# Kernel optimization log

Measured on AMD Instinct MI355X. Metric: run time of the kernel, lower is better.

## Reference

```python
import jax, jax.numpy as jnp
import numpy as np

N_CONTEXT = 8
N_ANS = 8


def _g_mlp(x, Wg1, bg1, Wg2, bg2, Wg3, bg3):
    # 3-layer relation MLP G, applied per object pair
    h = jax.nn.relu(x @ Wg1 + bg1)
    h = jax.nn.relu(h @ Wg2 + bg2)
    return jax.nn.relu(h @ Wg3 + bg3)


def setup_inputs() -> dict:
    key = jax.random.key(0)
    ks = jax.random.split(key, 12)
    B, P, C, H, W = 512, 16, 1, 80, 80
    D = 512                      # embedding_dim
    T = 2 * (D + 9)              # object_tuple_size = 1042
    s = jnp.float32(0.02)
    f32 = jnp.float32
    return {
        "x": jax.random.normal(ks[0], (B, P, C, H, W), f32),
        "W_emb": jax.random.normal(ks[1], (C * H * W, D), f32) * s,
        "b_emb": jnp.zeros((D,), f32),
        "Wg1": jax.random.normal(ks[2], (T, T), f32) * s,
        "bg1": jnp.zeros((T,), f32),
        "Wg2": jax.random.normal(ks[3], (T, T), f32) * s,
        "bg2": jnp.zeros((T,), f32),
        "Wg3": jax.random.normal(ks[4], (T, T), f32) * s,
        "bg3": jnp.zeros((T,), f32),
        "Wf1": jax.random.normal(ks[5], (T, T), f32) * s,
        "bf1": jnp.zeros((T,), f32),
        "Wf2": jax.random.normal(ks[6], (T, 1), f32) * s,
        "bf2": jnp.zeros((1,), f32),
        "labels_idx": jax.random.randint(ks[7], (B,), 0, N_ANS),
    }


def reference(x, W_emb, b_emb, Wg1, bg1, Wg2, bg2, Wg3, bg3,
              Wf1, bf1, Wf2, bf2, labels_idx):
    B = x.shape[0]
    D = W_emb.shape[1]
    # frozen embedding (torch.no_grad) -> stop_gradient
    emb = jax.lax.stop_gradient(
        x.reshape(B * (N_CONTEXT + N_ANS), -1) @ W_emb + b_emb
    ).reshape(B, N_CONTEXT + N_ANS, D)

    # TagPanelEmbeddings: context panels -> one-hot 0..7, answers -> one-hot 8 (9 dims)
    eye9 = jnp.eye(9, dtype=emb.dtype)
    tags = jnp.concatenate([eye9[:N_CONTEXT],
                            jnp.tile(eye9[8:9], (N_ANS, 1))], axis=0)  # (16, 9)
    tagged = jnp.concatenate(
        [emb, jnp.broadcast_to(tags, (B, N_CONTEXT + N_ANS, 9))], axis=-1)  # (B,16,D+9)

    ctx = tagged[:, :N_CONTEXT]   # (B,8,d)
    cho = tagged[:, N_CONTEXT:]   # (B,8,d)
    d = ctx.shape[-1]

    # all 8x8 ordered context pairs: pair[i,j] = concat(obj_j, obj_i)
    ctx_pairs = jnp.concatenate([
        jnp.broadcast_to(ctx[:, None, :, :], (B, 8, 8, d)),
        jnp.broadcast_to(ctx[:, :, None, :], (B, 8, 8, d)),
    ], axis=-1).reshape(B, 64, 2 * d)
    ctx_g = _g_mlp(ctx_pairs, Wg1, bg1, Wg2, bg2, Wg3, bg3).sum(axis=1)  # (B,T)

    # context-choice pairs, vectorized over all 8 answers:
    # pair[a,k] = concat(context_k, choice_a)  -> (B, N_ANS, 8, 2d)
    cc_pairs = jnp.concatenate([
        jnp.broadcast_to(ctx[:, None, :, :], (B, N_ANS, 8, d)),
        jnp.broadcast_to(cho[:, :, None, :], (B, N_ANS, 8, d)),
    ], axis=-1)
    cc_g = _g_mlp(cc_pairs, Wg1, bg1, Wg2, bg2, Wg3, bg3).sum(axis=2)  # (B,N_ANS,T)

    relations = ctx_g[:, None, :] + cc_g  # (B,N_ANS,T); norm = Identity

    # F readout: 2-layer MLP to scalar per answer
    h = jax.nn.relu(relations @ Wf1 + bf1)
    f_out = (h @ Wf2 + bf2)[..., 0]  # (B, N_ANS)

    labels = jax.nn.one_hot(labels_idx, N_ANS, dtype=f_out.dtype)
    # stable BCE-with-logits, mean over all elements
    loss = jnp.mean(jnp.maximum(f_out, 0) - f_out * labels
                    + jnp.log1p(jnp.exp(-jnp.abs(f_out))))
    preds = jnp.argmax(f_out, axis=1)
    acc = jnp.mean((preds == labels_idx).astype(f_out.dtype))
    return loss, acc
```

## Files before the change

### kernel.cpp

```cpp
#include <hip/hip_runtime.h>
#include <hip/hip_bf16.h>
#include <math.h>


typedef __bf16 bf16;
typedef __bf16 v8bf __attribute__((ext_vector_type(8)));
typedef float  v4f  __attribute__((ext_vector_type(4)));
typedef unsigned long long u64;

#define GAS(p) ((const __attribute__((address_space(1))) void*)(p))
#define LAS(p) ((__attribute__((address_space(3))) void*)(p))

__global__ __launch_bounds__(256) void gemm_bf16(
    const bf16* __restrict__ A, int lda,
    const bf16* __restrict__ Bt, int ldb,
    bf16* __restrict__ C, int ldc,
    int Mt, int Nt,
    int Nreal, int Nstore, int K,
    const float* __restrict__ bias,
    const float* __restrict__ tagW, int tag_ld,
    int relu, int mode)
{
    __shared__ bf16 As[128 * 32];
    __shared__ bf16 Bs[128 * 32];
    __shared__ bf16 Epi[64 * 132];

    const int L    = blockIdx.x;
    const int xcd  = L & 7;
    const int idx  = L >> 3;
    const int mlee = idx / Nt;
    const int n    = idx - mlee * Nt;
    const int m    = xcd * (Mt >> 3) + mlee;
    const int row0 = m * 128;
    const int col0 = n * 128;

    const int tid  = threadIdx.x;
    const int wv   = tid >> 6;
    const int lane = tid & 63;
    const int quad = lane >> 4;
    const int l15  = lane & 15;
    const int wm0  = (wv >> 1) * 64;
    const int wn0  = (wv & 1) * 64;

    v4f acc[4][4] = {};

    const int srow  = wv * 32 + (lane >> 2);
    const int skoff = (lane & 3) * 8;
    const bf16* ga = A  + (size_t)(row0 + srow) * lda + skoff;
    const bf16* gb = Bt + (size_t)(col0 + srow) * ldb + skoff;
    bf16* laA = &As[(wv * 32) * 32];
    bf16* laB = &Bs[(wv * 32) * 32];

    for (int k0 = 0; k0 < K; k0 += 32) {
        __builtin_amdgcn_global_load_lds(GAS(ga),                    LAS(laA),           16, 0, 0);
        __builtin_amdgcn_global_load_lds(GAS(ga + (size_t)16 * lda), LAS(laA + 16 * 32), 16, 0, 0);
        __builtin_amdgcn_global_load_lds(GAS(gb),                    LAS(laB),           16, 0, 0);
        __builtin_amdgcn_global_load_lds(GAS(gb + (size_t)16 * ldb), LAS(laB + 16 * 32), 16, 0, 0);
        ga += 32; gb += 32;
        __syncthreads();

        v8bf af[4], bfq[4];
        #pragma unroll
        for (int i = 0; i < 4; ++i)
            af[i] = *(const v8bf*)&As[(wm0 + i * 16 + l15) * 32 + quad * 8];
        #pragma unroll
        for (int j = 0; j < 4; ++j)
            bfq[j] = *(const v8bf*)&Bs[(wn0 + j * 16 + l15) * 32 + quad * 8];
        #pragma unroll
        for (int i = 0; i < 4; ++i)
            #pragma unroll
            for (int j = 0; j < 4; ++j)
                acc[i][j] = __builtin_amdgcn_mfma_f32_16x16x32_bf16(af[i], bfq[j], acc[i][j], 0, 0, 0);
        __syncthreads();
    }

    float bcol[4];
    #pragma unroll
    for (int j = 0; j < 4; ++j) {
        int col = col0 + wn0 + j * 16 + l15;
        bcol[j] = (col < Nreal && bias) ? bias[col] : 0.f;
    }

    float s_ctx = 0.f;

    #pragma unroll
    for (int pass = 0; pass < 2; ++pass) {
        if (wm0 == pass * 64) {
            #pragma unroll
            for (int i = 0; i < 4; ++i) {
                #pragma unroll
                for (int j = 0; j < 4; ++j) {
                    #pragma unroll
                    for (int r = 0; r < 4; ++r) {
                        int lrow = i * 16 + quad * 4 + r;
                        int lcol = wn0 + j * 16 + l15;
                        int col  = col0 + lcol;
                        float v = 0.f;
                        if (col < Nreal) {
                            v = acc[i][j][r] + bcol[j];
                            if (tagW) {
                                int row = row0 + pass * 64 + lrow;
                                int tp = row & 15; if (tp > 8) tp = 8;
                                v += tagW[(size_t)tp * tag_ld + col];
                            }
                            if (relu) v = fmaxf(v, 0.f);
                        }
                        Epi[lrow * 132 + lcol] = (bf16)v;
                    }
                }
            }
        }
        __syncthreads();

        if (mode == 0) {
            int lrow = tid >> 2;
            int cg   = (tid & 3) * 32;
            int grow = row0 + pass * 64 + lrow;
            #pragma unroll
            for (int k = 0; k < 4; ++k) {
                int c = cg + k * 8;
                int gcol = col0 + c;
                if (gcol < Nstore) {
                    u64 q0 = *(const u64*)&Epi[lrow * 132 + c];
                    u64 q1 = *(const u64*)&Epi[lrow * 132 + c + 4];
                    uint4 st;
                    st.x = (unsigned)q0; st.y = (unsigned)(q0 >> 32);
                    st.z = (unsigned)q1; st.w = (unsigned)(q1 >> 32);
                    *(uint4*)&C[(size_t)grow * ldc + gcol] = st;
                }
            }
        } else {
            if (tid < 128) {
                int col = tid;
                if (pass == 0) {
                    float s = 0.f;
                    for (int r = 0; r < 64; ++r) s += (float)Epi[r * 132 + col];
                    s_ctx = s;
                } else {
                    float sA[8] = {};
                    for (int r = 0; r < 64; ++r) sA[r >> 3] += (float)Epi[r * 132 + col];
                    int gcol = col0 + col;
                    if (gcol < Nstore) {
                        #pragma unroll
                        for (int a = 0; a < 8; ++a)
                            C[(size_t)(m * 8 + a) * ldc + gcol] = (bf16)(s_ctx + sA[a]);
                    }
                }
            }
        }
        __syncthreads();
    }
}

__global__ __launch_bounds__(512, 2) void gemm256(
    const bf16* __restrict__ A, int lda,
    const bf16* __restrict__ Bt, int ldb,
    bf16* __restrict__ C, int ldc,
    int Mt, int Nt, int Nreal, int Nstore, int K,
    const float* __restrict__ bias, int relu, int mode)
{
    extern __shared__ char smem[];
    (void)relu;

    const int NTK = K >> 6;

    const int L    = blockIdx.x;
    const int xcd  = L & 7;
    const int idx  = L >> 3;
    const int mlee = idx / Nt;
    const int n    = idx - mlee * Nt;
    const int m    = xcd * (Mt >> 3) + mlee;
    const int row0 = m * 256;
    const int col0 = n * 256;

    const int tid  = threadIdx.x;
    const int wv   = tid >> 6;
    const int lane = tid & 63;
    const int wr   = wv >> 2;
    const int wc   = wv & 3;
    const int l15  = lane & 15;
    const int quad = lane >> 4;
    const int s7   = l15 & 7;
    const int slot0 = ((0 + quad) ^ s7) << 4;
    const int slot1 = ((4 + quad) ^ s7) << 4;

    char* const aB0 = smem + wr * 16384;
    char* const bB0 = smem + 65536 + (wc >> 1) * 16384 + (wc & 1) * 8192;

    const int srow = tid >> 3;
    const int gce  = ((tid ^ srow) & 7) * 8;
    const bf16* const Ab = A  + (size_t)(row0 + srow) * lda + gce;
    const bf16* const Bb = Bt + (size_t)(col0 + srow) * ldb + gce;
    char* const ldsA = smem + wv * 1024;
    char* const ldsB = smem + 65536 + wv * 1024;

#define STAGE_A(kt, h, buf) { \
    const bf16* s0_ = Ab + (size_t)((h) * 128) * lda + (kt) * 64; \
    char* d_ = ldsA + (buf) * 32768 + (h) * 16384; \
    __builtin_amdgcn_global_load_lds(GAS(s0_),                    LAS(d_),        16, 0, 0); \
    __builtin_amdgcn_global_load_lds(GAS(s0_ + (size_t)64 * lda), LAS(d_ + 8192), 16, 0, 0); }
#define STAGE_B(kt, h, buf) { \
    const bf16* s0_ = Bb + (size_t)((h) * 128) * ldb + (kt) * 64; \
    char* d_ = ldsB + (buf) * 32768 + (h) * 16384; \
    __builtin_amdgcn_global_load_lds(GAS(s0_),                    LAS(d_),        16, 0, 0); \
    __builtin_amdgcn_global_load_lds(GAS(s0_ + (size_t)64 * ldb), LAS(d_ + 8192), 16, 0, 0); }

#define LDA4(buf, qmB) \
    _Pragma("unroll") \
    for (int i_ = 0; i_ < 4; ++i_) { \
        afr[i_][0] = *(const v8bf*)(aB0 + (buf) * 32768 + (((qmB) + i_) * 16 + l15) * 128 + slot0); \
        afr[i_][1] = *(const v8bf*)(aB0 + (buf) * 32768 + (((qmB) + i_) * 16 + l15) * 128 + slot1); \
    }
#define LDB2(buf, nfB) \
    _Pragma("unroll") \
    for (int j_ = 0; j_ < 2; ++j_) { \
        bfr[j_][0] = *(const v8bf*)(bB0 + (buf) * 32768 + (((nfB) + j_) * 16 + l15) * 128 + slot0); \
        bfr[j_][1] = *(const v8bf*)(bB0 + (buf) * 32768 + (((nfB) + j_) * 16 + l15) * 128 + slot1); \
    }
#define MM8(qmB, nfB) \
    _Pragma("unroll") \
    for (int i_ = 0; i_ < 4; ++i_) \
        _Pragma("unroll") \
        for (int j_ = 0; j_ < 2; ++j_) { \
            acc[(qmB) + i_][(nfB) + j_] = __builtin_amdgcn_mfma_f32_16x16x32_bf16(afr[i_][0], bfr[j_][0], acc[(qmB) + i_][(nfB) + j_], 0, 0, 0); \
            acc[(qmB) + i_][(nfB) + j_] = __builtin_amdgcn_mfma_f32_16x16x32_bf16(afr[i_][1], bfr[j_][1], acc[(qmB) + i_][(nfB) + j_], 0, 0, 0); \
        }
#define BAR()   asm volatile("s_barrier" ::: "memory")
#define PRIO1() __builtin_amdgcn_s_setprio(1)
#define PRIO0() __builtin_amdgcn_s_setprio(0)

    v4f acc[8][4] = {};
    v8bf afr[4][2], bfr[2][2];

    STAGE_A(0, 0, 0); STAGE_A(0, 1, 0); STAGE_B(0, 0, 0); STAGE_B(0, 1, 0);
    if (NTK > 1) {
        STAGE_A(1, 0, 1);
        asm volatile("s_waitcnt vmcnt(2)" ::: "memory");
    } else {
        asm volatile("s_waitcnt vmcnt(0)" ::: "memory");
    }
    BAR();

    int t = 0;
    for (; t + 1 < NTK; t += 2) {
        LDA4(0, 0); LDB2(0, 0); STAGE_A(t + 1, 1, 1);
        BAR(); PRIO1(); MM8(0, 0); PRIO0(); BAR();
        LDB2(0, 2); STAGE_B(t + 1, 0, 1);
        BAR(); PRIO1(); MM8(0, 2); PRIO0(); BAR();
        LDA4(0, 4); LDB2(0, 0); STAGE_B(t + 1, 1, 1);
        BAR(); PRIO1(); MM8(4, 0); PRIO0(); BAR();
        LDB2(0, 2);
        if (t + 2 < NTK) STAGE_A(t + 2, 0, 0);
        BAR(); PRIO1(); MM8(4, 2); PRIO0();
        if (t + 2 < NTK) asm volatile("s_waitcnt vmcnt(2)" ::: "memory");
        else             asm volatile("s_waitcnt vmcnt(0)" ::: "memory");
        BAR();
        LDA4(1, 0); LDB2(1, 0);
        if (t + 2 < NTK) STAGE_A(t + 2, 1, 0);
        BAR(); PRIO1(); MM8(0, 0); PRIO0(); BAR();
        LDB2(1, 2);
        if (t + 2 < NTK) STAGE_B(t + 2, 0, 0);
        BAR(); PRIO1(); MM8(0, 2); PRIO0(); BAR();
        LDA4(1, 4); LDB2(1, 0);
        if (t + 2 < NTK) STAGE_B(t + 2, 1, 0);
        BAR(); PRIO1(); MM8(4, 0); PRIO0(); BAR();
        LDB2(1, 2);
        if (t + 3 < NTK) STAGE_A(t + 3, 0, 1);
        BAR(); PRIO1(); MM8(4, 2); PRIO0();
        if (t + 3 < NTK) asm volatile("s_waitcnt vmcnt(2)" ::: "memory");
        else             asm volatile("s_waitcnt vmcnt(0)" ::: "memory");
        BAR();
    }
    if (t < NTK) {
        LDA4(0, 0); LDB2(0, 0); BAR(); PRIO1(); MM8(0, 0); PRIO0(); BAR();
        LDB2(0, 2);             BAR(); PRIO1(); MM8(0, 2); PRIO0(); BAR();
        LDA4(0, 4); LDB2(0, 0); BAR(); PRIO1(); MM8(4, 0); PRIO0(); BAR();
        LDB2(0, 2);             BAR(); PRIO1(); MM8(4, 2); PRIO0();
    }

    const int crow = row0 + wr * 128 + quad * 4;
    const int ccol = col0 + wc * 64 + l15;

    if (mode == 0) {
        #pragma unroll
        for (int j = 0; j < 4; ++j) {
            int col = ccol + j * 16;
            if (col < Nstore) {
                bool real = col < Nreal;
                float bc = (real && bias) ? bias[col] : 0.f;
                #pragma unroll
                for (int i = 0; i < 8; ++i) {
                    #pragma unroll
                    for (int r = 0; r < 4; ++r) {
                        float v = 0.f;
                        if (real) v = fmaxf(acc[i][j][r] + bc, 0.f);
                        C[(size_t)(crow + i * 16 + r) * ldc + col] = (bf16)v;
                    }
                }
            }
        }
    } else {
        const int bb = (row0 >> 7) + wr;
        #pragma unroll
        for (int j = 0; j < 4; ++j) {
            int col = ccol + j * 16;
            bool real = col < Nreal;
            float bc = (real && bias) ? bias[col] : 0.f;
            float red[9];
            float sc = 0.f;
            #pragma unroll
            for (int i = 0; i < 4; ++i)
                #pragma unroll
                for (int r = 0; r < 4; ++r)
                    sc += fmaxf(acc[i][j][r] + bc, 0.f);
            red[0] = sc;
            #pragma unroll
            for (int a = 0; a < 8; ++a) {
                float s = 0.f;
                if ((quad >> 1) == (a & 1)) {
                    const int i = 4 + (a >> 1);
                    #pragma unroll
                    for (int r = 0; r < 4; ++r)
                        s += fmaxf(acc[i][j][r] + bc, 0.f);
                }
                red[1 + a] = s;
            }
            #pragma unroll
            for (int k = 0; k < 9; ++k) {
                red[k] += __shfl_xor(red[k], 16, 64);
                red[k] += __shfl_xor(red[k], 32, 64);
            }
            if (quad == 0 && col < Nstore) {
                #pragma unroll
                for (int a = 0; a < 8; ++a)
                    C[(size_t)(bb * 8 + a) * ldc + col] = (bf16)(red[0] + red[1 + a]);
            }
        }
    }
#undef STAGE_A
#undef STAGE_B
#undef LDA4
#undef LDB2
#undef MM8
#undef BAR
#undef PRIO1
#undef PRIO0
}

__global__ void transpose_cast(const float* __restrict__ W, int ldw,
                               int krows, int ncols,
                               bf16* __restrict__ Bt, int ldb,
                               int nalloc, int kalloc)
{
    __shared__ float t[32][33];
    int kb = blockIdx.x * 32;
    int nb = blockIdx.y * 32;
    int tx = threadIdx.x, ty = threadIdx.y;
    #pragma unroll
    for (int i = 0; i < 4; ++i) {
        int k = kb + ty + i * 8, n = nb + tx;
        t[ty + i * 8][tx] = (k < krows && n < ncols) ? W[(size_t)k * ldw + n] : 0.f;
    }
    __syncthreads();
    #pragma unroll
    for (int i = 0; i < 4; ++i) {
        int n = nb + ty + i * 8, k = kb + tx;
        if (n < nalloc && k < kalloc)
            Bt[(size_t)n * ldb + k] = (bf16)t[tx][ty + i * 8];
    }
}

__global__ void cast_bf16_vec(const float* __restrict__ in, bf16* __restrict__ out, size_t n4)
{
    size_t i = blockIdx.x * (size_t)blockDim.x + threadIdx.x;
    if (i >= n4) return;
    float4 v = ((const float4*)in)[i];
    union { bf16 h[4]; u64 q; } o;
    o.h[0] = (bf16)v.x; o.h[1] = (bf16)v.y; o.h[2] = (bf16)v.z; o.h[3] = (bf16)v.w;
    *(u64*)&out[i * 4] = o.q;
}

__global__ void pair_build(const bf16* __restrict__ U, const bf16* __restrict__ V,
                           bf16* __restrict__ H1, int ldp)
{
    int r = blockIdx.x;
    int p = r & 127, bb = r >> 7;
    const bf16* ur = U + (size_t)(bb * 16 + (p & 7)) * ldp;
    const bf16* vr = V + (size_t)(bb * 16 + (p >> 3)) * ldp;
    bf16* hr = H1 + (size_t)r * ldp;
    int nch = ldp >> 3;
    for (int c8 = threadIdx.x; c8 < nch; c8 += blockDim.x) {
        v8bf u = *(const v8bf*)&ur[c8 * 8];
        v8bf v = *(const v8bf*)&vr[c8 * 8];
        v8bf o;
        #pragma unroll
        for (int i = 0; i < 8; ++i)
            o[i] = (bf16)fmaxf((float)u[i] + (float)v[i], 0.f);
        *(v8bf*)&hr[c8 * 8] = o;
    }
}

__global__ void fout_kernel(const bf16* __restrict__ h, const float* __restrict__ Wf2,
                            const float* __restrict__ bf2, float* __restrict__ fout,
                            int rows, int T, int ldp)
{
    int wid  = (int)((blockIdx.x * (size_t)blockDim.x + threadIdx.x) >> 6);
    int lane = threadIdx.x & 63;
    if (wid >= rows) return;
    const bf16* hr = h + (size_t)wid * ldp;
    float s = 0.f;
    for (int c = lane; c < T; c += 64) s += (float)hr[c] * Wf2[c];
    #pragma unroll
    for (int off = 32; off > 0; off >>= 1) s += __shfl_down(s, off, 64);
    if (lane == 0) fout[wid] = s + bf2[0];
}

__global__ void loss_kernel(const float* __restrict__ fout, const int* __restrict__ labels,
                            float* __restrict__ out)
{
    __shared__ float sl[512];
    __shared__ float sc[512];
    int b = threadIdx.x;
    const float* f = fout + (size_t)b * 8;
    int lab = labels[b];
    float rl = 0.f;
    int best = 0;
    float bv = f[0];
    #pragma unroll
    for (int a = 0; a < 8; ++a) {
        float v = f[a];
        rl += fmaxf(v, 0.f) - v * ((a == lab) ? 1.f : 0.f) + log1pf(expf(-fabsf(v)));
        if (v > bv) { bv = v; best = a; }
    }
    sl[b] = rl;
    sc[b] = (best == lab) ? 1.f : 0.f;
    __syncthreads();
    for (int s = 256; s > 0; s >>= 1) {
        if (b < s) { sl[b] += sl[b + s]; sc[b] += sc[b + s]; }
        __syncthreads();
    }
    if (b == 0) { out[0] = sl[0] / 4096.f; out[1] = sc[0] / 512.f; }
}

extern "C" void kernel_launch(void* const* d_in, const int* in_sizes, int n_in,
                              void* d_out, int out_size, void* d_ws, size_t ws_size,
                              hipStream_t stream)
{
    (void)in_sizes; (void)n_in; (void)out_size;
    const float* x      = (const float*)d_in[0];
    const float* W_emb  = (const float*)d_in[1];
    const float* b_emb  = (const float*)d_in[2];
    const float* Wg1    = (const float*)d_in[3];
    const float* bg1    = (const float*)d_in[4];
    const float* Wg2    = (const float*)d_in[5];
    const float* bg2    = (const float*)d_in[6];
    const float* Wg3    = (const float*)d_in[7];
    const float* bg3    = (const float*)d_in[8];
    const float* Wf1    = (const float*)d_in[9];
    const float* bf1    = (const float*)d_in[10];
    const float* Wf2    = (const float*)d_in[11];
    const float* bf2    = (const float*)d_in[12];
    const int*   labels = (const int*)d_in[13];

    const int B = 512, S = 16, E = 6400, D = 512, T = 1042;
    const int TP  = 1088;
    const int NA  = 1152;
    const int NAB = 1280;

    static int attr_set = 0;
    if (!attr_set) {
        (void)hipFuncSetAttribute((const void*)gemm256,
                                  hipFuncAttributeMaxDynamicSharedMemorySize, 131072);
        attr_set = 1;
    }

    auto alignup = [](size_t v) { return (v + 255) & ~(size_t)255; };

    size_t fixed = alignup((size_t)B * 8 * 4)
                 + alignup((size_t)D * E * 2)
                 + 2 * alignup((size_t)NA * D * 2)
                 + 2 * alignup((size_t)NAB * TP * 2)
                 + alignup((size_t)NA * TP * 2);

    int Bc = 512;
    for (;;) {
        size_t need = fixed
            + alignup((size_t)Bc * S * E * 2)
            + alignup((size_t)Bc * S * D * 2)
            + 2 * alignup((size_t)Bc * S * TP * 2)
            + 2 * alignup((size_t)Bc * 128 * TP * 2)
            + alignup((size_t)Bc * 8 * TP * 2)
            + alignup((size_t)Bc * 8 * TP * 2);
        if (need <= ws_size || Bc == 16) break;
        Bc >>= 1;
    }

    char* p = (char*)d_ws;
    auto take = [&](size_t bytes) -> void* {
        char* r = p; p += (bytes + 255) & ~(size_t)255; return r;
    };
    float* fout  = (float*)take((size_t)B * 8 * 4);
    bf16* W_embT = (bf16*)take((size_t)D * E * 2);
    bf16* W1aT   = (bf16*)take((size_t)NA * D * 2);
    bf16* W1bT   = (bf16*)take((size_t)NA * D * 2);
    bf16* Wg2T   = (bf16*)take((size_t)NAB * TP * 2);
    bf16* Wg3T   = (bf16*)take((size_t)NAB * TP * 2);
    bf16* Wf1T   = (bf16*)take((size_t)NA * TP * 2);
    bf16* xb     = (bf16*)take((size_t)Bc * S * E * 2);
    bf16* embB   = (bf16*)take((size_t)Bc * S * D * 2);
    bf16* Ubuf   = (bf16*)take((size_t)Bc * S * TP * 2);
    bf16* Vbuf   = (bf16*)take((size_t)Bc * S * TP * 2);
    bf16* H1     = (bf16*)take((size_t)Bc * 128 * TP * 2);
    bf16* H2     = (bf16*)take((size_t)Bc * 128 * TP * 2);
    bf16* REL    = (bf16*)take((size_t)Bc * 8 * TP * 2);
    bf16* HF     = (bf16*)take((size_t)Bc * 8 * TP * 2);

    dim3 tb(32, 8);
    transpose_cast<<<dim3(E / 32, D / 32), tb, 0, stream>>>(W_emb, D, E, D, W_embT, E, D, E);
    transpose_cast<<<dim3(D / 32, NA / 32), tb, 0, stream>>>(Wg1,                   T, D, T, W1aT, D, NA, D);
    transpose_cast<<<dim3(D / 32, NA / 32), tb, 0, stream>>>(Wg1 + (size_t)521 * T, T, D, T, W1bT, D, NA, D);
    transpose_cast<<<dim3(TP / 32, NAB / 32), tb, 0, stream>>>(Wg2, T, T, T, Wg2T, TP, NAB, TP);
    transpose_cast<<<dim3(TP / 32, NAB / 32), tb, 0, stream>>>(Wg3, T, T, T, Wg3T, TP, NAB, TP);
    transpose_cast<<<dim3(TP / 32, NA / 32), tb, 0, stream>>>(Wf1, T, T, T, Wf1T, TP, NA, TP);

    const int nch = B / Bc;
    for (int ch = 0; ch < nch; ++ch) {
        const int M1t = Bc * S / 128, M3t = Bc * 8 / 128;
        const int M2t6 = Bc * 128 / 256;

        size_t nx4 = (size_t)Bc * S * E / 4;
        cast_bf16_vec<<<(int)((nx4 + 255) / 256), 256, 0, stream>>>(
            x + (size_t)ch * Bc * S * E, xb, nx4);

        gemm_bf16<<<M1t * (D / 128), 256, 0, stream>>>(
            xb, E, W_embT, E, embB, D, M1t, D / 128, D, D, E, b_emb, nullptr, 0, 0, 0);

        gemm_bf16<<<M1t * (NA / 128), 256, 0, stream>>>(
            embB, D, W1aT, D, Ubuf, TP, M1t, NA / 128, T, TP, D, bg1, Wg1 + (size_t)512 * T, T, 0, 0);
        gemm_bf16<<<M1t * (NA / 128), 256, 0, stream>>>(
            embB, D, W1bT, D, Vbuf, TP, M1t, NA / 128, T, TP, D, nullptr, Wg1 + (size_t)1033 * T, T, 0, 0);

        pair_build<<<Bc * 128, 128, 0, stream>>>(Ubuf, Vbuf, H1, TP);

        gemm256<<<M2t6 * (NAB / 256), 512, 131072, stream>>>(
            H1, TP, Wg2T, TP, H2, TP, M2t6, NAB / 256, T, TP, TP, bg2, 1, 0);
        gemm256<<<M2t6 * (NAB / 256), 512, 131072, stream>>>(
            H2, TP, Wg3T, TP, REL, TP, M2t6, NAB / 256, T, TP, TP, bg3, 1, 1);

        gemm_bf16<<<M3t * (NA / 128), 256, 0, stream>>>(
            REL, TP, Wf1T, TP, HF, TP, M3t, NA / 128, T, TP, TP, bf1, nullptr, 0, 1, 0);

        fout_kernel<<<(Bc * 8 * 64 + 255) / 256, 256, 0, stream>>>(
            HF, Wf2, bf2, fout + (size_t)ch * Bc * 8, Bc * 8, T, TP);
    }

    loss_kernel<<<1, 512, 0, stream>>>(fout, labels, (float*)d_out);
}
```

Before: 1.049 ms.

## Fuse pair construction into layer-2 GEMM A-operand loading and stage epilogue via LDS

Removes the separate pair_build kernel and its materialized H1 buffer by having the layer-2 GEMM gather U and V rows from global memory, add them, apply ReLU, and write the result into swizzled LDS as the A tile. The K loop is restructured from a two-step unrolled double buffer into a single-step loop with a full vmcnt/lgkmcnt fence per iteration. The mode-0 epilogue now stages results through LDS for vectorized 16-byte global stores. This saves a large write and read of the pair tensor, at the cost of register-path A loads, extra VALU work inside the GEMM, and a stricter per-iteration fence.

```diff
diff --git a/kernel.cpp b/kernel.cpp
--- a/kernel.cpp
+++ b/kernel.cpp
@@ -152,15 +152,16 @@
     }
 }
 
+template<int AMODE, int CMODE>
 __global__ __launch_bounds__(512, 2) void gemm256(
     const bf16* __restrict__ A, int lda,
+    const bf16* __restrict__ U, const bf16* __restrict__ V, int lduv,
     const bf16* __restrict__ Bt, int ldb,
     bf16* __restrict__ C, int ldc,
     int Mt, int Nt, int Nreal, int Nstore, int K,
-    const float* __restrict__ bias, int relu, int mode)
+    const float* __restrict__ bias)
 {
     extern __shared__ char smem[];
-    (void)relu;
 
     const int NTK = K >> 6;
 
@@ -184,122 +185,152 @@
     const int slot0 = ((0 + quad) ^ s7) << 4;
     const int slot1 = ((4 + quad) ^ s7) << 4;
 
-    char* const aB0 = smem + wr * 16384;
-    char* const bB0 = smem + 65536 + (wc >> 1) * 16384 + (wc & 1) * 8192;
+    char* const aRd = smem + wr * 16384;
+    char* const bRd = smem + 65536 + (wc >> 1) * 16384 + (wc & 1) * 8192;
 
     const int srow = tid >> 3;
-    const int gce  = ((tid ^ srow) & 7) * 8;
-    const bf16* const Ab = A  + (size_t)(row0 + srow) * lda + gce;
+    const int sl   = tid & 7;
+    const int gce  = (sl ^ (srow & 7)) * 8;
+    const bf16* const Ab = (AMODE == 0 ? A : U) + (size_t)(row0 + srow) * (AMODE == 0 ? lda : 0) + gce;
     const bf16* const Bb = Bt + (size_t)(col0 + srow) * ldb + gce;
-    char* const ldsA = smem + wv * 1024;
-    char* const ldsB = smem + 65536 + wv * 1024;
-
-#define STAGE_A(kt, h, buf) { \
-    const bf16* s0_ = Ab + (size_t)((h) * 128) * lda + (kt) * 64; \
-    char* d_ = ldsA + (buf) * 32768 + (h) * 16384; \
-    __builtin_amdgcn_global_load_lds(GAS(s0_),                    LAS(d_),        16, 0, 0); \
-    __builtin_amdgcn_global_load_lds(GAS(s0_ + (size_t)64 * lda), LAS(d_ + 8192), 16, 0, 0); }
-#define STAGE_B(kt, h, buf) { \
-    const bf16* s0_ = Bb + (size_t)((h) * 128) * ldb + (kt) * 64; \
-    char* d_ = ldsB + (buf) * 32768 + (h) * 16384; \
-    __builtin_amdgcn_global_load_lds(GAS(s0_),                    LAS(d_),        16, 0, 0); \
-    __builtin_amdgcn_global_load_lds(GAS(s0_ + (size_t)64 * ldb), LAS(d_ + 8192), 16, 0, 0); }
-
-#define LDA4(buf, qmB) \
+
+#define STAGE_A(kt, bo, h) { \
+    const bf16* s_ = Ab + (size_t)((h) * 128) * lda + (kt) * 64; \
+    char* d_ = smem + (bo) + (h) * 16384 + wv * 1024; \
+    __builtin_amdgcn_global_load_lds(GAS(s_),                    LAS(d_),        16, 0, 0); \
+    __builtin_amdgcn_global_load_lds(GAS(s_ + (size_t)64 * lda), LAS(d_ + 8192), 16, 0, 0); }
+#define STAGE_B(kt, bo, h) { \
+    const bf16* s_ = Bb + (size_t)((h) * 128) * ldb + (kt) * 64; \
+    char* d_ = smem + 65536 + (bo) + (h) * 16384 + wv * 1024; \
+    __builtin_amdgcn_global_load_lds(GAS(s_),                    LAS(d_),        16, 0, 0); \
+    __builtin_amdgcn_global_load_lds(GAS(s_ + (size_t)64 * ldb), LAS(d_ + 8192), 16, 0, 0); }
+
+#define LDA4(bo, qmB) \
     _Pragma("unroll") \
     for (int i_ = 0; i_ < 4; ++i_) { \
-        afr[i_][0] = *(const v8bf*)(aB0 + (buf) * 32768 + (((qmB) + i_) * 16 + l15) * 128 + slot0); \
-        afr[i_][1] = *(const v8bf*)(aB0 + (buf) * 32768 + (((qmB) + i_) * 16 + l15) * 128 + slot1); \
-    }
-#define LDB2(buf, nfB) \
+        afr[i_][0] = *(const v8bf*)(aRd + (bo) + (((qmB) + i_) * 16 + l15) * 128 + slot0); \
+        afr[i_][1] = *(const v8bf*)(aRd + (bo) + (((qmB) + i_) * 16 + l15) * 128 + slot1); \
+    }
+#define LDB2(bo, nfB) \
     _Pragma("unroll") \
     for (int j_ = 0; j_ < 2; ++j_) { \
-        bfr[j_][0] = *(const v8bf*)(bB0 + (buf) * 32768 + (((nfB) + j_) * 16 + l15) * 128 + slot0); \
-        bfr[j_][1] = *(const v8bf*)(bB0 + (buf) * 32768 + (((nfB) + j_) * 16 + l15) * 128 + slot1); \
-    }
-#define MM8(qmB, nfB) \
+        bfr[(nfB) + j_][0] = *(const v8bf*)(bRd + (bo) + (((nfB) + j_) * 16 + l15) * 128 + slot0); \
+        bfr[(nfB) + j_][1] = *(const v8bf*)(bRd + (bo) + (((nfB) + j_) * 16 + l15) * 128 + slot1); \
+    }
+#define MM8(qmA, nfB) \
     _Pragma("unroll") \
     for (int i_ = 0; i_ < 4; ++i_) \
         _Pragma("unroll") \
         for (int j_ = 0; j_ < 2; ++j_) { \
-            acc[(qmB) + i_][(nfB) + j_] = __builtin_amdgcn_mfma_f32_16x16x32_bf16(afr[i_][0], bfr[j_][0], acc[(qmB) + i_][(nfB) + j_], 0, 0, 0); \
-            acc[(qmB) + i_][(nfB) + j_] = __builtin_amdgcn_mfma_f32_16x16x32_bf16(afr[i_][1], bfr[j_][1], acc[(qmB) + i_][(nfB) + j_], 0, 0, 0); \
-        }
+            acc[(qmA) + i_][(nfB) + j_] = __builtin_amdgcn_mfma_f32_16x16x32_bf16(afr[i_][0], bfr[(nfB) + j_][0], acc[(qmA) + i_][(nfB) + j_], 0, 0, 0); \
+            acc[(qmA) + i_][(nfB) + j_] = __builtin_amdgcn_mfma_f32_16x16x32_bf16(afr[i_][1], bfr[(nfB) + j_][1], acc[(qmA) + i_][(nfB) + j_], 0, 0, 0); \
+        }
+#define UVLOAD(uu, vv, h, t1) { \
+    uu[0] = *(const v8bf*)(U + uo[h][0] + (t1) * 64); \
+    vv[0] = *(const v8bf*)(V + vo[h][0] + (t1) * 64); \
+    uu[1] = *(const v8bf*)(U + uo[h][1] + (t1) * 64); \
+    vv[1] = *(const v8bf*)(V + vo[h][1] + (t1) * 64); }
+#define WRITEA(uu, vv, bo, h) { \
+    _Pragma("unroll") \
+    for (int q_ = 0; q_ < 2; ++q_) { \
+        v8bf o_; \
+        _Pragma("unroll") \
+        for (int e_ = 0; e_ < 8; ++e_) \
+            o_[e_] = (bf16)fmaxf((float)uu[q_][e_] + (float)vv[q_][e_], 0.f); \
+        *(v8bf*)(smem + (bo) + (h) * 16384 + (q_ * 64 + srow) * 128 + ((sl ^ (srow & 7)) << 4)) = o_; \
+    } }
 #define BAR()   asm volatile("s_barrier" ::: "memory")
+#define FENCE() asm volatile("s_waitcnt vmcnt(0) lgkmcnt(0)" ::: "memory")
 #define PRIO1() __builtin_amdgcn_s_setprio(1)
 #define PRIO0() __builtin_amdgcn_s_setprio(0)
 
     v4f acc[8][4] = {};
-    v8bf afr[4][2], bfr[2][2];
-
-    STAGE_A(0, 0, 0); STAGE_A(0, 1, 0); STAGE_B(0, 0, 0); STAGE_B(0, 1, 0);
-    if (NTK > 1) {
-        STAGE_A(1, 0, 1);
-        asm volatile("s_waitcnt vmcnt(2)" ::: "memory");
+    v8bf afr[4][2], bfr[4][2];
+    v8bf u0[2], v0[2], u1[2], v1[2];
+    int uo[2][2], vo[2][2];
+
+    if constexpr (AMODE == 1) {
+        #pragma unroll
+        for (int h = 0; h < 2; ++h)
+            #pragma unroll
+            for (int q = 0; q < 2; ++q) {
+                int gr = row0 + h * 128 + q * 64 + srow;
+                int bb = gr >> 7, p = gr & 127;
+                uo[h][q] = (bb * 16 + (p & 7)) * lduv + sl * 8;
+                vo[h][q] = (bb * 16 + (p >> 3)) * lduv + sl * 8;
+            }
+    }
+
+    if constexpr (AMODE == 0) {
+        STAGE_A(0, 0, 0); STAGE_A(0, 0, 1);
     } else {
-        asm volatile("s_waitcnt vmcnt(0)" ::: "memory");
-    }
+        UVLOAD(u0, v0, 0, 0); UVLOAD(u1, v1, 1, 0);
+    }
+    STAGE_B(0, 0, 0); STAGE_B(0, 0, 1);
+    if constexpr (AMODE == 1) {
+        WRITEA(u0, v0, 0, 0); WRITEA(u1, v1, 0, 1);
+    }
+    FENCE();
     BAR();
 
-    int t = 0;
-    for (; t + 1 < NTK; t += 2) {
-        LDA4(0, 0); LDB2(0, 0); STAGE_A(t + 1, 1, 1);
+    for (int t = 0; t < NTK; ++t) {
+        const int bo = (t & 1) << 15;
+        const int no = bo ^ 32768;
+        const bool hn = (t + 1 < NTK);
+        LDA4(bo, 0); LDB2(bo, 0);
+        if constexpr (AMODE == 0) { if (hn) STAGE_A(t + 1, no, 0); }
         BAR(); PRIO1(); MM8(0, 0); PRIO0(); BAR();
-        LDB2(0, 2); STAGE_B(t + 1, 0, 1);
+        LDB2(bo, 2);
+        if (hn) {
+            if constexpr (AMODE == 1) { UVLOAD(u0, v0, 0, t + 1); }
+            else                      { STAGE_A(t + 1, no, 1); }
+            STAGE_B(t + 1, no, 0);
+        }
         BAR(); PRIO1(); MM8(0, 2); PRIO0(); BAR();
-        LDA4(0, 4); LDB2(0, 0); STAGE_B(t + 1, 1, 1);
+        LDA4(bo, 4);
+        if (hn) {
+            if constexpr (AMODE == 1) { UVLOAD(u1, v1, 1, t + 1); WRITEA(u0, v0, no, 0); }
+            STAGE_B(t + 1, no, 1);
+        }
         BAR(); PRIO1(); MM8(4, 0); PRIO0(); BAR();
-        LDB2(0, 2);
-        if (t + 2 < NTK) STAGE_A(t + 2, 0, 0);
-        BAR(); PRIO1(); MM8(4, 2); PRIO0();
-        if (t + 2 < NTK) asm volatile("s_waitcnt vmcnt(2)" ::: "memory");
-        else             asm volatile("s_waitcnt vmcnt(0)" ::: "memory");
-        BAR();
-        LDA4(1, 0); LDB2(1, 0);
-        if (t + 2 < NTK) STAGE_A(t + 2, 1, 0);
-        BAR(); PRIO1(); MM8(0, 0); PRIO0(); BAR();
-        LDB2(1, 2);
-        if (t + 2 < NTK) STAGE_B(t + 2, 0, 0);
-        BAR(); PRIO1(); MM8(0, 2); PRIO0(); BAR();
-        LDA4(1, 4); LDB2(1, 0);
-        if (t + 2 < NTK) STAGE_B(t + 2, 1, 0);
-        BAR(); PRIO1(); MM8(4, 0); PRIO0(); BAR();
-        LDB2(1, 2);
-        if (t + 3 < NTK) STAGE_A(t + 3, 0, 1);
-        BAR(); PRIO1(); MM8(4, 2); PRIO0();
-        if (t + 3 < NTK) asm volatile("s_waitcnt vmcnt(2)" ::: "memory");
-        else             asm volatile("s_waitcnt vmcnt(0)" ::: "memory");
-        BAR();
-    }
-    if (t < NTK) {
-        LDA4(0, 0); LDB2(0, 0); BAR(); PRIO1(); MM8(0, 0); PRIO0(); BAR();
-        LDB2(0, 2);             BAR(); PRIO1(); MM8(0, 2); PRIO0(); BAR();
-        LDA4(0, 4); LDB2(0, 0); BAR(); PRIO1(); MM8(4, 0); PRIO0(); BAR();
-        LDB2(0, 2);             BAR(); PRIO1(); MM8(4, 2); PRIO0();
-    }
-
-    const int crow = row0 + wr * 128 + quad * 4;
-    const int ccol = col0 + wc * 64 + l15;
-
-    if (mode == 0) {
+        if (hn) {
+            if constexpr (AMODE == 1) { WRITEA(u1, v1, no, 1); }
+        }
+        FENCE();
+        BAR(); PRIO1(); MM8(4, 2); PRIO0(); BAR();
+    }
+
+    if constexpr (CMODE == 0) {
+        __syncthreads();
+        bf16* epi = (bf16*)(smem + wv * 16384);
         #pragma unroll
         for (int j = 0; j < 4; ++j) {
-            int col = ccol + j * 16;
-            if (col < Nstore) {
-                bool real = col < Nreal;
-                float bc = (real && bias) ? bias[col] : 0.f;
+            int col = col0 + wc * 64 + j * 16 + l15;
+            bool real = col < Nreal;
+            float bc = (real && bias) ? bias[col] : 0.f;
+            #pragma unroll
+            for (int i = 0; i < 8; ++i) {
                 #pragma unroll
-                for (int i = 0; i < 8; ++i) {
-                    #pragma unroll
-                    for (int r = 0; r < 4; ++r) {
-                        float v = 0.f;
-                        if (real) v = fmaxf(acc[i][j][r] + bc, 0.f);
-                        C[(size_t)(crow + i * 16 + r) * ldc + col] = (bf16)v;
-                    }
+                for (int r = 0; r < 4; ++r) {
+                    int lrow = i * 16 + quad * 4 + r;
+                    float v = real ? fmaxf(acc[i][j][r] + bc, 0.f) : 0.f;
+                    int slt = (j * 2 + (l15 >> 3)) ^ (lrow & 7);
+                    epi[(lrow * 128 + (slt << 4) + ((l15 & 7) << 1)) >> 1] = (bf16)v;
                 }
             }
         }
+        #pragma unroll
+        for (int it = 0; it < 16; ++it) {
+            int lrow = it * 8 + (lane >> 3);
+            int cb   = lane & 7;
+            v8bf vv = *(const v8bf*)&epi[(lrow * 128 + ((cb ^ (lrow & 7)) << 4)) >> 1];
+            int grow = row0 + wr * 128 + lrow;
+            int gcol = col0 + wc * 64 + cb * 8;
+            if (gcol < Nstore)
+                *(v8bf*)&C[(size_t)grow * ldc + gcol] = vv;
+        }
     } else {
+        const int ccol = col0 + wc * 64 + l15;
         const int bb = (row0 >> 7) + wr;
         #pragma unroll
         for (int j = 0; j < 4; ++j) {
@@ -342,7 +373,10 @@
 #undef LDA4
 #undef LDB2
 #undef MM8
+#undef UVLOAD
+#undef WRITEA
 #undef BAR
+#undef FENCE
 #undef PRIO1
 #undef PRIO0
 }
@@ -378,26 +412,6 @@
     union { bf16 h[4]; u64 q; } o;
     o.h[0] = (bf16)v.x; o.h[1] = (bf16)v.y; o.h[2] = (bf16)v.z; o.h[3] = (bf16)v.w;
     *(u64*)&out[i * 4] = o.q;
-}
-
-__global__ void pair_build(const bf16* __restrict__ U, const bf16* __restrict__ V,
-                           bf16* __restrict__ H1, int ldp)
-{
-    int r = blockIdx.x;
-    int p = r & 127, bb = r >> 7;
-    const bf16* ur = U + (size_t)(bb * 16 + (p & 7)) * ldp;
-    const bf16* vr = V + (size_t)(bb * 16 + (p >> 3)) * ldp;
-    bf16* hr = H1 + (size_t)r * ldp;
-    int nch = ldp >> 3;
-    for (int c8 = threadIdx.x; c8 < nch; c8 += blockDim.x) {
-        v8bf u = *(const v8bf*)&ur[c8 * 8];
-        v8bf v = *(const v8bf*)&vr[c8 * 8];
-        v8bf o;
-        #pragma unroll
-        for (int i = 0; i < 8; ++i)
-            o[i] = (bf16)fmaxf((float)u[i] + (float)v[i], 0.f);
-        *(v8bf*)&hr[c8 * 8] = o;
-    }
 }
 
 __global__ void fout_kernel(const bf16* __restrict__ h, const float* __restrict__ Wf2,
@@ -469,7 +483,9 @@
 
     static int attr_set = 0;
     if (!attr_set) {
-        (void)hipFuncSetAttribute((const void*)gemm256,
+        (void)hipFuncSetAttribute(reinterpret_cast<const void*>(&gemm256<1, 0>),
+                                  hipFuncAttributeMaxDynamicSharedMemorySize, 131072);
+        (void)hipFuncSetAttribute(reinterpret_cast<const void*>(&gemm256<0, 1>),
                                   hipFuncAttributeMaxDynamicSharedMemorySize, 131072);
         attr_set = 1;
     }
@@ -488,7 +504,7 @@
             + alignup((size_t)Bc * S * E * 2)
             + alignup((size_t)Bc * S * D * 2)
             + 2 * alignup((size_t)Bc * S * TP * 2)
-            + 2 * alignup((size_t)Bc * 128 * TP * 2)
+            + alignup((size_t)Bc * 128 * TP * 2)
             + alignup((size_t)Bc * 8 * TP * 2)
             + alignup((size_t)Bc * 8 * TP * 2);
         if (need <= ws_size || Bc == 16) break;
@@ -510,7 +526,6 @@
     bf16* embB   = (bf16*)take((size_t)Bc * S * D * 2);
     bf16* Ubuf   = (bf16*)take((size_t)Bc * S * TP * 2);
     bf16* Vbuf   = (bf16*)take((size_t)Bc * S * TP * 2);
-    bf16* H1     = (bf16*)take((size_t)Bc * 128 * TP * 2);
     bf16* H2     = (bf16*)take((size_t)Bc * 128 * TP * 2);
     bf16* REL    = (bf16*)take((size_t)Bc * 8 * TP * 2);
     bf16* HF     = (bf16*)take((size_t)Bc * 8 * TP * 2);
@@ -540,12 +555,10 @@
         gemm_bf16<<<M1t * (NA / 128), 256, 0, stream>>>(
             embB, D, W1bT, D, Vbuf, TP, M1t, NA / 128, T, TP, D, nullptr, Wg1 + (size_t)1033 * T, T, 0, 0);
 
-        pair_build<<<Bc * 128, 128, 0, stream>>>(Ubuf, Vbuf, H1, TP);
-
-        gemm256<<<M2t6 * (NAB / 256), 512, 131072, stream>>>(
-            H1, TP, Wg2T, TP, H2, TP, M2t6, NAB / 256, T, TP, TP, bg2, 1, 0);
-        gemm256<<<M2t6 * (NAB / 256), 512, 131072, stream>>>(
-            H2, TP, Wg3T, TP, REL, TP, M2t6, NAB / 256, T, TP, TP, bg3, 1, 1);
+        gemm256<1, 0><<<M2t6 * (NAB / 256), 512, 131072, stream>>>(
+            nullptr, 0, Ubuf, Vbuf, TP, Wg2T, TP, H2, TP, M2t6, NAB / 256, T, TP, TP, bg2);
+        gemm256<0, 1><<<M2t6 * (NAB / 256), 512, 131072, stream>>>(
+            H2, TP, nullptr, nullptr, 0, Wg3T, TP, REL, TP, M2t6, NAB / 256, T, TP, TP, bg3);
 
         gemm_bf16<<<M3t * (NA / 128), 256, 0, stream>>>(
             REL, TP, Wf1T, TP, HF, TP, M3t, NA / 128, T, TP, TP, bf1, nullptr, 0, 1, 0);
```

New measurement: 1.152 ms. 1.1x slower.

## Merge U/V layer-1 GEMMs into one wide GEMM and stage gemm256 epilogue via LDS

Applied to the files above, without the earlier changes.

The two first-layer GEMMs that produced the U and V halves are merged into a single GEMM with a concatenated transposed weight (2304 columns). A new build_tag kernel precomputes a combined tag/bias table that feeds that GEMM's tag input, and pair_build reads both halves from the one UV buffer. Separately, the gemm256 mode-0 epilogue now writes results through a swizzled shared-memory tile so each lane stores 16-byte row-contiguous vectors instead of scattered 2-byte values. The aim is fewer launches and better-coalesced global stores, at the cost of an extra barrier and LDS traffic in the epilogue.

```diff
diff --git a/kernel.cpp b/kernel.cpp
--- a/kernel.cpp
+++ b/kernel.cpp
@@ -278,26 +278,36 @@
         LDB2(0, 2);             BAR(); PRIO1(); MM8(4, 2); PRIO0();
     }
 
-    const int crow = row0 + wr * 128 + quad * 4;
     const int ccol = col0 + wc * 64 + l15;
 
     if (mode == 0) {
+        __syncthreads();
+        bf16* epi = (bf16*)(smem + wv * 16384);
         #pragma unroll
         for (int j = 0; j < 4; ++j) {
             int col = ccol + j * 16;
-            if (col < Nstore) {
-                bool real = col < Nreal;
-                float bc = (real && bias) ? bias[col] : 0.f;
+            bool real = col < Nreal;
+            float bc = (real && bias) ? bias[col] : 0.f;
+            #pragma unroll
+            for (int i = 0; i < 8; ++i) {
                 #pragma unroll
-                for (int i = 0; i < 8; ++i) {
-                    #pragma unroll
-                    for (int r = 0; r < 4; ++r) {
-                        float v = 0.f;
-                        if (real) v = fmaxf(acc[i][j][r] + bc, 0.f);
-                        C[(size_t)(crow + i * 16 + r) * ldc + col] = (bf16)v;
-                    }
+                for (int r = 0; r < 4; ++r) {
+                    int lrow = i * 16 + quad * 4 + r;
+                    float v = real ? fmaxf(acc[i][j][r] + bc, 0.f) : 0.f;
+                    int slt = (j * 2 + (l15 >> 3)) ^ (lrow & 7);
+                    epi[(lrow * 128 + (slt << 4) + ((l15 & 7) << 1)) >> 1] = (bf16)v;
                 }
             }
+        }
+        #pragma unroll
+        for (int it = 0; it < 16; ++it) {
+            int lrow = it * 8 + (lane >> 3);
+            int cb   = lane & 7;
+            v8bf vv = *(const v8bf*)&epi[(lrow * 128 + ((cb ^ (lrow & 7)) << 4)) >> 1];
+            int grow = row0 + wr * 128 + lrow;
+            int gcol = col0 + wc * 64 + cb * 8;
+            if (gcol < Nstore)
+                *(v8bf*)&C[(size_t)grow * ldc + gcol] = vv;
         }
     } else {
         const int bb = (row0 >> 7) + wr;
@@ -380,13 +390,29 @@
     *(u64*)&out[i * 4] = o.q;
 }
 
-__global__ void pair_build(const bf16* __restrict__ U, const bf16* __restrict__ V,
+__global__ void build_tag(const float* __restrict__ Wg1, const float* __restrict__ bg1,
+                          float* __restrict__ TAG, int T, int D, int half, int W)
+{
+    int i = blockIdx.x * blockDim.x + threadIdx.x;
+    if (i >= 9 * W) return;
+    int tp = i / W, c = i % W;
+    float v = 0.f;
+    if (c < half) {
+        if (c < T) v = Wg1[(size_t)(D + tp) * T + c] + bg1[c];
+    } else {
+        int cc = c - half;
+        if (cc < T) v = Wg1[(size_t)(2 * D + 9 + tp) * T + cc];
+    }
+    TAG[i] = v;
+}
+
+__global__ void pair_build(const bf16* __restrict__ UV, int lduv, int voff,
                            bf16* __restrict__ H1, int ldp)
 {
     int r = blockIdx.x;
     int p = r & 127, bb = r >> 7;
-    const bf16* ur = U + (size_t)(bb * 16 + (p & 7)) * ldp;
-    const bf16* vr = V + (size_t)(bb * 16 + (p >> 3)) * ldp;
+    const bf16* ur = UV + (size_t)(bb * 16 + (p & 7)) * lduv;
+    const bf16* vr = UV + (size_t)(bb * 16 + (p >> 3)) * lduv + voff;
     bf16* hr = H1 + (size_t)r * ldp;
     int nch = ldp >> 3;
     for (int c8 = threadIdx.x; c8 < nch; c8 += blockDim.x) {
@@ -466,10 +492,11 @@
     const int TP  = 1088;
     const int NA  = 1152;
     const int NAB = 1280;
+    const int NA2 = 2304;
 
     static int attr_set = 0;
     if (!attr_set) {
-        (void)hipFuncSetAttribute((const void*)gemm256,
+        (void)hipFuncSetAttribute(reinterpret_cast<const void*>(&gemm256),
                                   hipFuncAttributeMaxDynamicSharedMemorySize, 131072);
         attr_set = 1;
     }
@@ -478,16 +505,17 @@
 
     size_t fixed = alignup((size_t)B * 8 * 4)
                  + alignup((size_t)D * E * 2)
-                 + 2 * alignup((size_t)NA * D * 2)
+                 + alignup((size_t)NA2 * D * 2)
                  + 2 * alignup((size_t)NAB * TP * 2)
-                 + alignup((size_t)NA * TP * 2);
+                 + alignup((size_t)NA * TP * 2)
+                 + alignup((size_t)9 * NA2 * 4);
 
     int Bc = 512;
     for (;;) {
         size_t need = fixed
             + alignup((size_t)Bc * S * E * 2)
             + alignup((size_t)Bc * S * D * 2)
-            + 2 * alignup((size_t)Bc * S * TP * 2)
+            + alignup((size_t)Bc * S * NA2 * 2)
             + 2 * alignup((size_t)Bc * 128 * TP * 2)
             + alignup((size_t)Bc * 8 * TP * 2)
             + alignup((size_t)Bc * 8 * TP * 2);
@@ -501,15 +529,14 @@
     };
     float* fout  = (float*)take((size_t)B * 8 * 4);
     bf16* W_embT = (bf16*)take((size_t)D * E * 2);
-    bf16* W1aT   = (bf16*)take((size_t)NA * D * 2);
-    bf16* W1bT   = (bf16*)take((size_t)NA * D * 2);
+    bf16* W1abT  = (bf16*)take((size_t)NA2 * D * 2);
     bf16* Wg2T   = (bf16*)take((size_t)NAB * TP * 2);
     bf16* Wg3T   = (bf16*)take((size_t)NAB * TP * 2);
     bf16* Wf1T   = (bf16*)take((size_t)NA * TP * 2);
+    float* TAG   = (float*)take((size_t)9 * NA2 * 4);
     bf16* xb     = (bf16*)take((size_t)Bc * S * E * 2);
     bf16* embB   = (bf16*)take((size_t)Bc * S * D * 2);
-    bf16* Ubuf   = (bf16*)take((size_t)Bc * S * TP * 2);
-    bf16* Vbuf   = (bf16*)take((size_t)Bc * S * TP * 2);
+    bf16* UV     = (bf16*)take((size_t)Bc * S * NA2 * 2);
     bf16* H1     = (bf16*)take((size_t)Bc * 128 * TP * 2);
     bf16* H2     = (bf16*)take((size_t)Bc * 128 * TP * 2);
     bf16* REL    = (bf16*)take((size_t)Bc * 8 * TP * 2);
@@ -517,11 +544,12 @@
 
     dim3 tb(32, 8);
     transpose_cast<<<dim3(E / 32, D / 32), tb, 0, stream>>>(W_emb, D, E, D, W_embT, E, D, E);
-    transpose_cast<<<dim3(D / 32, NA / 32), tb, 0, stream>>>(Wg1,                   T, D, T, W1aT, D, NA, D);
-    transpose_cast<<<dim3(D / 32, NA / 32), tb, 0, stream>>>(Wg1 + (size_t)521 * T, T, D, T, W1bT, D, NA, D);
+    transpose_cast<<<dim3(D / 32, NA / 32), tb, 0, stream>>>(Wg1,                   T, D, T, W1abT, D, NA, D);
+    transpose_cast<<<dim3(D / 32, NA / 32), tb, 0, stream>>>(Wg1 + (size_t)521 * T, T, D, T, W1abT + (size_t)NA * D, D, NA, D);
     transpose_cast<<<dim3(TP / 32, NAB / 32), tb, 0, stream>>>(Wg2, T, T, T, Wg2T, TP, NAB, TP);
     transpose_cast<<<dim3(TP / 32, NAB / 32), tb, 0, stream>>>(Wg3, T, T, T, Wg3T, TP, NAB, TP);
     transpose_cast<<<dim3(TP / 32, NA / 32), tb, 0, stream>>>(Wf1, T, T, T, Wf1T, TP, NA, TP);
+    build_tag<<<(9 * NA2 + 255) / 256, 256, 0, stream>>>(Wg1, bg1, TAG, T, D, NA, NA2);
 
     const int nch = B / Bc;
     for (int ch = 0; ch < nch; ++ch) {
@@ -535,12 +563,11 @@
         gemm_bf16<<<M1t * (D / 128), 256, 0, stream>>>(
             xb, E, W_embT, E, embB, D, M1t, D / 128, D, D, E, b_emb, nullptr, 0, 0, 0);
 
-        gemm_bf16<<<M1t * (NA / 128), 256, 0, stream>>>(
-            embB, D, W1aT, D, Ubuf, TP, M1t, NA / 128, T, TP, D, bg1, Wg1 + (size_t)512 * T, T, 0, 0);
-        gemm_bf16<<<M1t * (NA / 128), 256, 0, stream>>>(
-            embB, D, W1bT, D, Vbuf, TP, M1t, NA / 128, T, TP, D, nullptr, Wg1 + (size_t)1033 * T, T, 0, 0);
-
-        pair_build<<<Bc * 128, 128, 0, stream>>>(Ubuf, Vbuf, H1, TP);
+        gemm_bf16<<<M1t * (NA2 / 128), 256, 0, stream>>>(
+            embB, D, W1abT, D, UV, NA2, M1t, NA2 / 128, NA2, NA2, D,
+            nullptr, TAG, NA2, 0, 0);
+
+        pair_build<<<Bc * 128, 128, 0, stream>>>(UV, NA2, NA, H1, TP);
 
         gemm256<<<M2t6 * (NAB / 256), 512, 131072, stream>>>(
             H1, TP, Wg2T, TP, H2, TP, M2t6, NAB / 256, T, TP, TP, bg2, 1, 0);
```

Measured after the change: 1.035 ms. Within noise of the previous version (-1.4%).
